# Kernel tuning notes

Measured on AMD Instinct MI355X. Metric: run time of the kernel, lower is better.

## Reference

```python
import jax, jax.numpy as jnp
import numpy as np

N, H, S = 2048, 512, 256

def setup_inputs() -> dict:
    key = jax.random.key(0)
    k1, k2, k3 = jax.random.split(key, 3)
    hidden_states = jax.random.normal(k1, (N, H, S), dtype=jnp.float32)
    # xavier_uniform-ish scale for W and context vector
    limW = float(np.sqrt(6.0 / (H + H)))
    attention_weights = jax.random.uniform(k2, (H, H), dtype=jnp.float32, minval=-limW, maxval=limW)
    attention_bias = jnp.zeros((H, 1), dtype=jnp.float32)
    limc = float(np.sqrt(6.0 / (H + 1)))
    context_vector = jax.random.uniform(k3, (H, 1), dtype=jnp.float32, minval=-limc, maxval=limc)
    return {
        "hidden_states": hidden_states,
        "attention_weights": attention_weights,
        "attention_bias": attention_bias,
        "context_vector": context_vector,
    }

def reference(hidden_states, attention_weights, attention_bias, context_vector):
    # hidden_states: (N, H, S)
    hs_t = jnp.swapaxes(hidden_states, 1, 2)              # (N, S, H)
    score = jnp.tanh(hs_t @ attention_weights + attention_bias[:, 0])  # (N, S, H)
    alignment = (score @ context_vector)[..., 0]          # (N, S)
    attn = jax.nn.softmax(alignment, axis=1)              # (N, S)
    context = jnp.einsum('ns,nhs->nh', attn, hidden_states)  # (N, H)
    return context
```

## Files before the change

kernel.cpp:

```cpp
#include <hip/hip_runtime.h>
#include <hip/hip_bf16.h>
#include <stdint.h>
#include <stddef.h>

typedef __attribute__((ext_vector_type(8))) short short8;
typedef __attribute__((ext_vector_type(4))) float f32x4;
typedef __attribute__((ext_vector_type(16))) float f32x16;

#define NB 2048
#define HD 512
#define SD 256

#define AROW 516

__device__ __forceinline__ short f2bf(float x) {
  __hip_bfloat16 h = __float2bfloat16(x);
  return *reinterpret_cast<short*>(&h);
}

__device__ __forceinline__ float fast_tanh(float x) {
  x = fminf(fmaxf(x, -15.f), 15.f);
  float e = __expf(2.f * x);
  return __fdividef(e - 1.f, e + 1.f);
}

__global__ __launch_bounds__(256) void wconv_kernel(const float* __restrict__ W,
                                                    short* __restrict__ Wtb16) {
  __shared__ float tile[32][33];
  const int bx = blockIdx.x;
  const int tk0 = (bx & 15) * 32;
  const int tj0 = (bx >> 4) * 32;
  const int lx = threadIdx.x & 31;
  const int ly = threadIdx.x >> 5;
  for (int r = 0; r < 4; ++r) {
    int yy = ly + r * 8;
    tile[yy][lx] = W[(size_t)(tk0 + yy) * HD + tj0 + lx];
  }
  __syncthreads();
  for (int r = 0; r < 4; ++r) {
    int yy = ly + r * 8;
    const int k = tk0 + lx;
    Wtb16[(size_t)(k >> 4) * (HD * 16) + (size_t)(tj0 + yy) * 16 + (k & 15)] =
        f2bf(tile[lx][yy]);
  }
}

__global__ void __launch_bounds__(512, 4)
align_kernel(const float* __restrict__ hs, const short* __restrict__ Wtb16,
             const float* __restrict__ bias, const float* __restrict__ ctxv,
             float* __restrict__ align_out)
{
  __shared__ short As[64 * AROW];
  __shared__ float abuf[64];

  const int tid = threadIdx.x;
  const int n = blockIdx.x >> 2;
  const int s0 = (blockIdx.x & 3) * 64;
  const float* hsn = hs + (size_t)n * (HD * SD) + s0;

  if (tid < 64) abuf[tid] = 0.f;

  {
    const int a_s = tid & 63;
    const int a_kg = tid >> 6;
    #pragma unroll
    for (int o = 0; o < 8; ++o) {
      const int k0 = a_kg * 64 + o * 8;
      const float* src = hsn + (size_t)k0 * SD + a_s;
      short8 pk;
      #pragma unroll
      for (int e = 0; e < 8; ++e) pk[e] = f2bf(src[(size_t)e * SD]);
      *(short8*)&As[a_s * AROW + k0] = pk;
    }
  }
  __syncthreads();

  const int lane = tid & 63;
  const int wid = tid >> 6;
  const int jb = wid * 64;
  const int l31 = lane & 31;
  const int hg = lane >> 5;

  f32x16 acc[2][2];
  #pragma unroll
  for (int i = 0; i < 2; ++i)
    #pragma unroll
    for (int p = 0; p < 2; ++p)
      #pragma unroll
      for (int q = 0; q < 16; ++q) acc[i][p][q] = 0.f;

  const short* wlane = Wtb16 + (size_t)(jb + l31) * 16 + hg * 8;
  const int afo = l31 * AROW + hg * 8;

  short8 wb[3][2];
  short8 ab[2][2];

  #pragma unroll
  for (int d = 0; d < 3; ++d) {
    const short* wk = wlane + (size_t)d * (HD * 16);
    wb[d][0] = *(const short8*)(wk);
    wb[d][1] = *(const short8*)(wk + 32 * 16);
  }
  #pragma unroll
  for (int d = 0; d < 2; ++d) {
    ab[d][0] = *(const short8*)&As[afo + d * 16];
    ab[d][1] = *(const short8*)&As[afo + 32 * AROW + d * 16];
  }

  #pragma unroll
  for (int kb = 0; kb < 32; ++kb) {
    const int ws = kb % 3;
    const int as = kb & 1;

    __builtin_amdgcn_s_setprio(1);
    acc[0][0] = __builtin_amdgcn_mfma_f32_32x32x16_bf16(wb[ws][0], ab[as][0], acc[0][0], 0, 0, 0);
    acc[0][1] = __builtin_amdgcn_mfma_f32_32x32x16_bf16(wb[ws][1], ab[as][0], acc[0][1], 0, 0, 0);
    acc[1][0] = __builtin_amdgcn_mfma_f32_32x32x16_bf16(wb[ws][0], ab[as][1], acc[1][0], 0, 0, 0);
    acc[1][1] = __builtin_amdgcn_mfma_f32_32x32x16_bf16(wb[ws][1], ab[as][1], acc[1][1], 0, 0, 0);
    __builtin_amdgcn_s_setprio(0);

    if (kb < 29) {
      const short* wk = wlane + (size_t)(kb + 3) * (HD * 16);
      wb[ws][0] = *(const short8*)(wk);
      wb[ws][1] = *(const short8*)(wk + 32 * 16);
    }
    if (kb < 30) {
      ab[as][0] = *(const short8*)&As[afo + (kb + 2) * 16];
      ab[as][1] = *(const short8*)&As[afo + 32 * AROW + (kb + 2) * 16];
    }
  }

  float part0 = 0.f, part1 = 0.f;
  #pragma unroll
  for (int p = 0; p < 2; ++p) {
    const int jfr = jb + p * 32 + hg * 4;
    #pragma unroll
    for (int g = 0; g < 4; ++g) {
      const int j4 = jfr + g * 8;
      f32x4 bv = *(const f32x4*)(bias + j4);
      f32x4 cv = *(const f32x4*)(ctxv + j4);
      #pragma unroll
      for (int r = 0; r < 4; ++r) {
        const int q = g * 4 + r;
        part0 += fast_tanh(acc[0][p][q] + bv[r]) * cv[r];
        part1 += fast_tanh(acc[1][p][q] + bv[r]) * cv[r];
      }
    }
  }
  part0 += __shfl_xor(part0, 32);
  part1 += __shfl_xor(part1, 32);
  if (lane < 32) {
    atomicAdd(&abuf[l31], part0);
    atomicAdd(&abuf[32 + l31], part1);
  }
  __syncthreads();
  if (tid < 64) align_out[(size_t)n * SD + s0 + tid] = abuf[tid];
}

__global__ __launch_bounds__(256) void ctx_kernel(const float* __restrict__ hs,
                                                  const float* __restrict__ align_in,
                                                  float* __restrict__ out)
{
  __shared__ __align__(16) float attn_s[256];
  __shared__ float red[8];
  const int n = blockIdx.x;
  const int t = threadIdx.x;
  const int lane = t & 63, wid = t >> 6;

  float a = align_in[(size_t)n * 256 + t];
  float m = a;
  #pragma unroll
  for (int off = 32; off; off >>= 1) m = fmaxf(m, __shfl_xor(m, off));
  if (lane == 0) red[wid] = m;
  __syncthreads();
  m = fmaxf(fmaxf(red[0], red[1]), fmaxf(red[2], red[3]));
  float e = __expf(a - m);
  float s = e;
  #pragma unroll
  for (int off = 32; off; off >>= 1) s += __shfl_xor(s, off);
  if (lane == 0) red[4 + wid] = s;
  __syncthreads();
  s = red[4] + red[5] + red[6] + red[7];
  attn_s[t] = e / s;
  __syncthreads();

  const int grp = t & 7;
  const int hrow = t >> 3;
  float av[32];
  #pragma unroll
  for (int u = 0; u < 8; ++u) {
    float4 v = *(const float4*)&attn_s[grp * 32 + u * 4];
    av[4*u+0] = v.x; av[4*u+1] = v.y; av[4*u+2] = v.z; av[4*u+3] = v.w;
  }
  const float* hb = hs + (size_t)n * (HD * SD) + grp * 32;
  for (int it = 0; it < 16; ++it) {
    const int h = it * 32 + hrow;
    const float4* p = (const float4*)(hb + (size_t)h * SD);
    float acc = 0.f;
    #pragma unroll
    for (int u = 0; u < 8; ++u) {
      float4 v = p[u];
      acc += av[4*u+0]*v.x + av[4*u+1]*v.y + av[4*u+2]*v.z + av[4*u+3]*v.w;
    }
    acc += __shfl_xor(acc, 1);
    acc += __shfl_xor(acc, 2);
    acc += __shfl_xor(acc, 4);
    if (grp == 0) out[(size_t)n * HD + h] = acc;
  }
}

extern "C" void kernel_launch(void* const* d_in, const int* in_sizes, int n_in,
                              void* d_out, int out_size, void* d_ws, size_t ws_size,
                              hipStream_t stream) {
  (void)in_sizes; (void)n_in; (void)out_size; (void)ws_size;
  const float* hs = (const float*)d_in[0];
  const float* W  = (const float*)d_in[1];
  const float* b  = (const float*)d_in[2];
  const float* c  = (const float*)d_in[3];
  float* out = (float*)d_out;

  float* align_ws = (float*)d_ws;
  short* Wtb16 = (short*)((char*)d_ws + (size_t)NB * SD * 4);

  wconv_kernel<<<256, 256, 0, stream>>>(W, Wtb16);
  align_kernel<<<NB * 4, 512, 0, stream>>>(hs, Wtb16, b, c, align_ws);
  ctx_kernel<<<NB, 256, 0, stream>>>(hs, align_ws, out);
}
```

Before: 681.8 us.

## Pipeline hidden-state staging into LDS across K chunks overlapping MFMA compute

The align kernel no longer loads and converts the whole 64x512 activation tile into LDS before computing. It stages the tile in four 128-wide K chunks, prefetching the next chunk's fp32 values into registers while MFMAs run on the current chunk, with a barrier after each chunk. The W prefetch depth drops from 3 to 2 and the occupancy hint drops from 4 to 2 blocks per CU to make room for the extra registers. The aim is to hide global load latency behind matrix math, at the cost of extra barriers and possibly lower occupancy.

```diff
diff --git a/kernel.cpp b/kernel.cpp
--- a/kernel.cpp
+++ b/kernel.cpp
@@ -45,7 +45,7 @@
   }
 }
 
-__global__ void __launch_bounds__(512, 4)
+__global__ void __launch_bounds__(512, 2)
 align_kernel(const float* __restrict__ hs, const short* __restrict__ Wtb16,
              const float* __restrict__ bias, const float* __restrict__ ctxv,
              float* __restrict__ align_out)
@@ -60,26 +60,41 @@
 
   if (tid < 64) abuf[tid] = 0.f;
 
-  {
-    const int a_s = tid & 63;
-    const int a_kg = tid >> 6;
-    #pragma unroll
-    for (int o = 0; o < 8; ++o) {
-      const int k0 = a_kg * 64 + o * 8;
-      const float* src = hsn + (size_t)k0 * SD + a_s;
-      short8 pk;
-      #pragma unroll
-      for (int e = 0; e < 8; ++e) pk[e] = f2bf(src[(size_t)e * SD]);
-      *(short8*)&As[a_s * AROW + k0] = pk;
-    }
-  }
-  __syncthreads();
+  const int a_s = tid & 63;
+  const int kbase = (tid >> 6) * 16;
+  const float* aSrc = hsn + a_s + (size_t)kbase * SD;
+  short* aDstRow = &As[a_s * AROW + kbase];
 
   const int lane = tid & 63;
   const int wid = tid >> 6;
   const int jb = wid * 64;
   const int l31 = lane & 31;
   const int hg = lane >> 5;
+  const short* wlane = Wtb16 + (size_t)(jb + l31) * 16 + hg * 8;
+  const int afo = l31 * AROW + hg * 8;
+
+  float ra[16];
+
+  #pragma unroll
+  for (int e = 0; e < 16; ++e) ra[e] = aSrc[(size_t)e * SD];
+
+  short8 wb[2][2];
+  wb[0][0] = *(const short8*)(wlane);
+  wb[0][1] = *(const short8*)(wlane + 32 * 16);
+  wb[1][0] = *(const short8*)(wlane + (size_t)(HD * 16));
+  wb[1][1] = *(const short8*)(wlane + (size_t)(HD * 16) + 32 * 16);
+
+  {
+    short8 pk0, pk1;
+    #pragma unroll
+    for (int e = 0; e < 8; ++e) { pk0[e] = f2bf(ra[e]); pk1[e] = f2bf(ra[8 + e]); }
+    *(short8*)(aDstRow) = pk0;
+    *(short8*)(aDstRow + 8) = pk1;
+  }
+  #pragma unroll
+  for (int e = 0; e < 16; ++e) ra[e] = aSrc[(size_t)(128 + e) * SD];
+
+  __syncthreads();
 
   f32x16 acc[2][2];
   #pragma unroll
@@ -89,44 +104,50 @@
       #pragma unroll
       for (int q = 0; q < 16; ++q) acc[i][p][q] = 0.f;
 
-  const short* wlane = Wtb16 + (size_t)(jb + l31) * 16 + hg * 8;
-  const int afo = l31 * AROW + hg * 8;
-
-  short8 wb[3][2];
-  short8 ab[2][2];
-
-  #pragma unroll
-  for (int d = 0; d < 3; ++d) {
-    const short* wk = wlane + (size_t)d * (HD * 16);
-    wb[d][0] = *(const short8*)(wk);
-    wb[d][1] = *(const short8*)(wk + 32 * 16);
-  }
-  #pragma unroll
-  for (int d = 0; d < 2; ++d) {
-    ab[d][0] = *(const short8*)&As[afo + d * 16];
-    ab[d][1] = *(const short8*)&As[afo + 32 * AROW + d * 16];
-  }
-
-  #pragma unroll
-  for (int kb = 0; kb < 32; ++kb) {
-    const int ws = kb % 3;
-    const int as = kb & 1;
-
-    __builtin_amdgcn_s_setprio(1);
-    acc[0][0] = __builtin_amdgcn_mfma_f32_32x32x16_bf16(wb[ws][0], ab[as][0], acc[0][0], 0, 0, 0);
-    acc[0][1] = __builtin_amdgcn_mfma_f32_32x32x16_bf16(wb[ws][1], ab[as][0], acc[0][1], 0, 0, 0);
-    acc[1][0] = __builtin_amdgcn_mfma_f32_32x32x16_bf16(wb[ws][0], ab[as][1], acc[1][0], 0, 0, 0);
-    acc[1][1] = __builtin_amdgcn_mfma_f32_32x32x16_bf16(wb[ws][1], ab[as][1], acc[1][1], 0, 0, 0);
-    __builtin_amdgcn_s_setprio(0);
-
-    if (kb < 29) {
-      const short* wk = wlane + (size_t)(kb + 3) * (HD * 16);
-      wb[ws][0] = *(const short8*)(wk);
-      wb[ws][1] = *(const short8*)(wk + 32 * 16);
-    }
-    if (kb < 30) {
-      ab[as][0] = *(const short8*)&As[afo + (kb + 2) * 16];
-      ab[as][1] = *(const short8*)&As[afo + 32 * AROW + (kb + 2) * 16];
+  #pragma unroll
+  for (int p = 0; p < 4; ++p) {
+    short8 ab[2][2];
+    ab[0][0] = *(const short8*)&As[afo + p * 128];
+    ab[0][1] = *(const short8*)&As[afo + 32 * AROW + p * 128];
+    ab[1][0] = *(const short8*)&As[afo + p * 128 + 16];
+    ab[1][1] = *(const short8*)&As[afo + 32 * AROW + p * 128 + 16];
+
+    #pragma unroll
+    for (int i = 0; i < 8; ++i) {
+      const int kb = p * 8 + i;
+      const int ws = kb & 1;
+      const int as_ = i & 1;
+
+      __builtin_amdgcn_s_setprio(1);
+      acc[0][0] = __builtin_amdgcn_mfma_f32_32x32x16_bf16(wb[ws][0], ab[as_][0], acc[0][0], 0, 0, 0);
+      acc[0][1] = __builtin_amdgcn_mfma_f32_32x32x16_bf16(wb[ws][1], ab[as_][0], acc[0][1], 0, 0, 0);
+      acc[1][0] = __builtin_amdgcn_mfma_f32_32x32x16_bf16(wb[ws][0], ab[as_][1], acc[1][0], 0, 0, 0);
+      acc[1][1] = __builtin_amdgcn_mfma_f32_32x32x16_bf16(wb[ws][1], ab[as_][1], acc[1][1], 0, 0, 0);
+      __builtin_amdgcn_s_setprio(0);
+
+      if (kb < 30) {
+        const short* wk = wlane + (size_t)(kb + 2) * (HD * 16);
+        wb[ws][0] = *(const short8*)(wk);
+        wb[ws][1] = *(const short8*)(wk + 32 * 16);
+      }
+      if (i < 6) {
+        ab[as_][0] = *(const short8*)&As[afo + p * 128 + (i + 2) * 16];
+        ab[as_][1] = *(const short8*)&As[afo + 32 * AROW + p * 128 + (i + 2) * 16];
+      }
+    }
+
+    if (p < 3) {
+      short8 pk0, pk1;
+      #pragma unroll
+      for (int e = 0; e < 8; ++e) { pk0[e] = f2bf(ra[e]); pk1[e] = f2bf(ra[8 + e]); }
+      *(short8*)(aDstRow + (p + 1) * 128) = pk0;
+      *(short8*)(aDstRow + (p + 1) * 128 + 8) = pk1;
+      if (p < 2) {
+        #pragma unroll
+        for (int e = 0; e < 16; ++e)
+          ra[e] = aSrc[(size_t)((p + 2) * 128 + e) * SD];
+      }
+      __syncthreads();
     }
   }
 
```

Result: slower. 802.5 us (+17.7%).
